# Performance work log

Hardware: AMD Instinct MI355X
Metric: run time of the kernel (lower is better)

The kernel has to match this reference:

```python
import jax, jax.numpy as jnp
import numpy as np

EPS = 1e-5
C_M, C, C_Z = 256, 32, 128
N_SEQ, N_RES = 256, 1024


def setup_inputs() -> dict:
    key = jax.random.key(0)
    k1, k2, k3 = jax.random.split(key, 3)
    msa = jax.random.normal(k1, (N_SEQ, N_RES, C_M), dtype=jnp.float32)
    norm_w = jnp.ones((C_M,), dtype=jnp.float32)
    norm_b = jnp.zeros((C_M,), dtype=jnp.float32)
    w_ab = jax.random.normal(k2, (C, C_M), dtype=jnp.float32) * (1.0 / np.sqrt(C_M))
    b_ab = jnp.zeros((C,), dtype=jnp.float32)
    w_out = jax.random.normal(k3, (C_Z, C * C), dtype=jnp.float32) * (1.0 / C)
    b_out = jnp.zeros((C_Z,), dtype=jnp.float32)
    return {"msa": msa, "norm_w": norm_w, "norm_b": norm_b,
            "w_ab": w_ab, "b_ab": b_ab, "w_out": w_out, "b_out": b_out}


def reference(msa, norm_w, norm_b, w_ab, b_ab, w_out, b_out):
    # msa: (s, r, c_m) -> (r, s, c_m)
    x = jnp.transpose(msa, (1, 0, 2))
    s = x.shape[1]
    # LayerNorm over c_m
    mu = jnp.mean(x, axis=-1, keepdims=True)
    var = jnp.mean(jnp.square(x - mu), axis=-1, keepdims=True)
    xn = (x - mu) * jax.lax.rsqrt(var + EPS) * norm_w + norm_b
    # a == b: same linear applied twice to same input in the original
    a = jnp.einsum('rsm,cm->rsc', xn, w_ab) + b_ab          # (r, s, c)
    # mean over s of outer product == batched A^T A / s  -> (r, c, c)
    o = jnp.einsum('rsx,rsy->rxy', a, a) / s
    o = o.reshape(o.shape[0], C * C)                        # (r, c*c)
    pre_pair = jnp.einsum('rk,zk->rz', o, w_out) + b_out    # (r, c_z)
    r = pre_pair.shape[0]
    # unsqueeze(1).expand(r, r, c_z)
    pair = jnp.broadcast_to(pre_pair[:, None, :], (r, r, C_Z))
    return pair
```

## Files before the change

kernel.cpp:

```cpp
#include <hip/hip_runtime.h>

#define NSEQ 256
#define NRES 1024
#define CM   256
#define CC   32
#define CZ   128
#define EPS  1e-5f
#define SROW (NRES * CM)

typedef float f4v __attribute__((ext_vector_type(4)));
typedef __attribute__((ext_vector_type(8))) short short8;
typedef __attribute__((ext_vector_type(4))) float f32x4;
typedef unsigned int u32;

__device__ __forceinline__ float trunc_bf16(float f) {
    return __uint_as_float(__float_as_uint(f) & 0xffff0000u);
}
__device__ __forceinline__ u32 pk_bf16(float a, float b) {
    return (__float_as_uint(b) & 0xffff0000u) | (__float_as_uint(a) >> 16);
}

__global__ void opm_setup(const float* __restrict__ nw,
                          const float* __restrict__ nb,
                          const float* __restrict__ w_ab,
                          const float* __restrict__ b_ab,
                          float* __restrict__ k12,
                          unsigned short* __restrict__ wb_su)
{
    __shared__ float wls[CM * CC];
    const int t = threadIdx.x;
    const float nwm = nw[t];
    #pragma unroll
    for (int c = 0; c < CC; ++c)
        wls[t * CC + c] = nwm * w_ab[c * CM + t];
    __syncthreads();
    if (t < CC) {
        float k1 = 0.f, k2 = 0.f;
        for (int m = 0; m < CM; ++m) {
            k1 += wls[m * CC + t];
            k2 = fmaf(nb[m], w_ab[t * CM + m], k2);
        }
        k12[t]      = k1;
        k12[CC + t] = k2 + b_ab[t];
    }
    for (int e = t; e < 16384; e += 256) {
        const int j     = e & 7;
        const int l     = (e >> 3) & 63;
        const int split = (e >> 9) & 1;
        const int nt    = (e >> 10) & 1;
        const int kk    = e >> 11;
        const int m = (kk << 5) + ((l >> 4) << 3) + j;
        const int c = (nt << 4) + (l & 15);
        const float w  = wls[m * CC + c];
        const float w1 = trunc_bf16(w);
        const float v  = split ? (w - w1) : w;
        wb_su[e] = (unsigned short)(__float_as_uint(v) >> 16);
    }
}

__launch_bounds__(256, 2)
__global__ void opm_compute(const float* __restrict__ msa,
                            const u32*  __restrict__ wb_g,
                            const float* __restrict__ k12,
                            const float* __restrict__ w_out,
                            const float* __restrict__ b_out,
                            float* __restrict__ pre_out)
{
    __shared__ u32 xp[2 * 5120];
    __shared__ u32 wbl[8192];
    __shared__ float st[520];

    const int tid = threadIdx.x;
    const int r   = blockIdx.x;
    const int w   = tid >> 6;
    const int l   = tid & 63;

    const int sc8 = tid & 7;
    const int sg8 = tid >> 3;
    const float* xr = msa + (size_t)r * CM + (sc8 << 2);

    u32* xp1 = xp;
    u32* xp2 = xp + 5120;

    #pragma unroll
    for (int k = 0; k < 8; ++k) {
        const int i = (tid + (k << 8)) << 2;
        *(f4v*)&wbl[i] = *(const f4v*)&wb_g[i];
    }

    f32x4 acc[4][2];
    #pragma unroll
    for (int mt = 0; mt < 4; ++mt) { acc[mt][0] = (f32x4)0.f; acc[mt][1] = (f32x4)0.f; }
    float psum[8], pssq[8];
    #pragma unroll
    for (int k = 0; k < 8; ++k) { psum[k] = 0.f; pssq[k] = 0.f; }

    float4 pf[8];
    #pragma unroll
    for (int k = 0; k < 8; ++k)
        pf[k] = *(const float4*)(xr + (size_t)(sg8 + (k << 5)) * SROW);

    for (int kk = 0; kk < 8; ++kk) {
        __syncthreads();
        #pragma unroll
        for (int k = 0; k < 8; ++k) {
            const float4 p = pf[k];
            const int row = sg8 + (k << 5);
            const u32 a0 = pk_bf16(p.x, p.y), a1 = pk_bf16(p.z, p.w);
            const float rx = p.x - trunc_bf16(p.x);
            const float ry = p.y - trunc_bf16(p.y);
            const float rz = p.z - trunc_bf16(p.z);
            const float rw = p.w - trunc_bf16(p.w);
            const u32 b0 = pk_bf16(rx, ry), b1 = pk_bf16(rz, rw);
            *(uint2*)&xp1[row * 20 + (sc8 << 1)] = make_uint2(a0, a1);
            *(uint2*)&xp2[row * 20 + (sc8 << 1)] = make_uint2(b0, b1);
            psum[k] += (p.x + p.y) + (p.z + p.w);
            pssq[k]  = fmaf(p.x, p.x, fmaf(p.y, p.y, fmaf(p.z, p.z, fmaf(p.w, p.w, pssq[k]))));
        }
        __syncthreads();
        if (kk < 7) {
            #pragma unroll
            for (int k = 0; k < 8; ++k)
                pf[k] = *(const float4*)(xr + (size_t)(sg8 + (k << 5)) * SROW + ((kk + 1) << 5));
        }
        short8 B[2][2];
        #pragma unroll
        for (int nt = 0; nt < 2; ++nt)
            #pragma unroll
            for (int sp = 0; sp < 2; ++sp) {
                const int fb = ((((kk << 1) + nt) << 1) + sp) * 256 + (l << 2);
                B[nt][sp] = __builtin_bit_cast(short8, *(const f4v*)&wbl[fb]);
            }
        #pragma unroll
        for (int mt = 0; mt < 4; ++mt) {
            const int arow = ((w << 6) + (mt << 4) + (l & 15)) * 20 + ((l >> 4) << 2);
            const short8 A1 = __builtin_bit_cast(short8, *(const f4v*)&xp1[arow]);
            const short8 A2 = __builtin_bit_cast(short8, *(const f4v*)&xp2[arow]);
            acc[mt][0] = __builtin_amdgcn_mfma_f32_16x16x32_bf16(A1, B[0][0], acc[mt][0], 0, 0, 0);
            acc[mt][1] = __builtin_amdgcn_mfma_f32_16x16x32_bf16(A1, B[1][0], acc[mt][1], 0, 0, 0);
            acc[mt][0] = __builtin_amdgcn_mfma_f32_16x16x32_bf16(A1, B[0][1], acc[mt][0], 0, 0, 0);
            acc[mt][1] = __builtin_amdgcn_mfma_f32_16x16x32_bf16(A1, B[1][1], acc[mt][1], 0, 0, 0);
            acc[mt][0] = __builtin_amdgcn_mfma_f32_16x16x32_bf16(A2, B[0][0], acc[mt][0], 0, 0, 0);
            acc[mt][1] = __builtin_amdgcn_mfma_f32_16x16x32_bf16(A2, B[1][0], acc[mt][1], 0, 0, 0);
        }
    }
    __syncthreads();

    #pragma unroll
    for (int k = 0; k < 8; ++k) {
        float s1 = psum[k], s2 = pssq[k];
        s1 += __shfl_xor(s1, 1); s1 += __shfl_xor(s1, 2); s1 += __shfl_xor(s1, 4);
        s2 += __shfl_xor(s2, 1); s2 += __shfl_xor(s2, 2); s2 += __shfl_xor(s2, 4);
        if (sc8 == 0) {
            const int s = sg8 + (k << 5);
            const float mu  = s1 * (1.f / CM);
            const float var = s2 * (1.f / CM) - mu * mu;
            st[s]        = mu;
            st[256 + s]  = 1.f / sqrtf(var + EPS);
        }
    }
    __syncthreads();

    float* aB = (float*)xp;
    {
        const int cl = l & 15;
        const float k1_0 = k12[cl],      k1_1 = k12[16 + cl];
        const float k2_0 = k12[CC + cl], k2_1 = k12[CC + 16 + cl];
        #pragma unroll
        for (int mt = 0; mt < 4; ++mt) {
            #pragma unroll
            for (int rg = 0; rg < 4; ++rg) {
                const int s = (w << 6) + (mt << 4) + ((l >> 4) << 2) + rg;
                const float mu = st[s], rs = st[256 + s];
                const float a0 = fmaf(rs, acc[mt][0][rg] - mu * k1_0, k2_0);
                const float a1 = fmaf(rs, acc[mt][1][rg] - mu * k1_1, k2_1);
                const int sw = s & 7;
                aB[s * CC + (((cl >> 2) ^ sw) << 2) + (cl & 3)]       = a0;
                aB[s * CC + ((((cl >> 2) + 4) ^ sw) << 2) + (cl & 3)] = a1;
            }
        }
    }
    __syncthreads();

    float* scr = (float*)wbl;
    const int grp = w;
    const int xs_ = (tid >> 3) & 7;
    const int ys_ = tid & 7;
    float4 pr0 = {0,0,0,0}, pr1 = {0,0,0,0}, pr2 = {0,0,0,0}, pr3 = {0,0,0,0};
    #pragma unroll 4
    for (int si = 0; si < 64; ++si) {
        const int s  = (grp << 6) + si;
        const int sw = s & 7;
        const float4 ax = *(const float4*)&aB[s * CC + ((xs_ ^ sw) << 2)];
        const float4 ay = *(const float4*)&aB[s * CC + ((ys_ ^ sw) << 2)];
        pr0.x = fmaf(ax.x, ay.x, pr0.x); pr0.y = fmaf(ax.x, ay.y, pr0.y);
        pr0.z = fmaf(ax.x, ay.z, pr0.z); pr0.w = fmaf(ax.x, ay.w, pr0.w);
        pr1.x = fmaf(ax.y, ay.x, pr1.x); pr1.y = fmaf(ax.y, ay.y, pr1.y);
        pr1.z = fmaf(ax.y, ay.z, pr1.z); pr1.w = fmaf(ax.y, ay.w, pr1.w);
        pr2.x = fmaf(ax.z, ay.x, pr2.x); pr2.y = fmaf(ax.z, ay.y, pr2.y);
        pr2.z = fmaf(ax.z, ay.z, pr2.z); pr2.w = fmaf(ax.z, ay.w, pr2.w);
        pr3.x = fmaf(ax.w, ay.x, pr3.x); pr3.y = fmaf(ax.w, ay.y, pr3.y);
        pr3.z = fmaf(ax.w, ay.z, pr3.z); pr3.w = fmaf(ax.w, ay.w, pr3.w);
    }
    {
        float* pb = &scr[(grp << 10) + ((xs_ << 2) * CC) + (ys_ << 2)];
        *(float4*)&pb[0 * CC] = pr0;
        *(float4*)&pb[1 * CC] = pr1;
        *(float4*)&pb[2 * CC] = pr2;
        *(float4*)&pb[3 * CC] = pr3;
    }
    __syncthreads();
    {
        const float inv_s = 1.f / NSEQ;
        float4 a4 = *(const float4*)&scr[(tid << 2)];
        const float4 b1 = *(const float4*)&scr[1024 + (tid << 2)];
        const float4 b2 = *(const float4*)&scr[2048 + (tid << 2)];
        const float4 b3 = *(const float4*)&scr[3072 + (tid << 2)];
        a4.x = (a4.x + b1.x + b2.x + b3.x) * inv_s;
        a4.y = (a4.y + b1.y + b2.y + b3.y) * inv_s;
        a4.z = (a4.z + b1.z + b2.z + b3.z) * inv_s;
        a4.w = (a4.w + b1.w + b2.w + b3.w) * inv_s;
        *(float4*)&scr[tid << 2] = a4;
    }
    __syncthreads();

    {
        const int z    = tid & 127;
        const int half = tid >> 7;
        const float* wrow = w_out + (size_t)z * (CC * CC) + half * 512;
        const float* op   = &scr[half * 512];
        float po = 0.f;
        #pragma unroll 8
        for (int k = 0; k < 512; k += 4) {
            const float4 o4 = *(const float4*)&op[k];
            const float4 w4 = *(const float4*)&wrow[k];
            po = fmaf(o4.x, w4.x, fmaf(o4.y, w4.y, fmaf(o4.z, w4.z, fmaf(o4.w, w4.w, po))));
        }
        scr[4096 + (half << 7) + z] = po;
    }
    __syncthreads();
    if (tid < CZ)
        pre_out[(size_t)r * CZ + tid] = scr[4096 + tid] + scr[4096 + CZ + tid] + b_out[tid];
}

__launch_bounds__(256, 8)
__global__ void opm_bcast(const float* __restrict__ pre,
                          float* __restrict__ out)
{
    const int bid = blockIdx.x;
    const int r   = bid >> 3;
    const int jb  = bid & 7;
    const int z4  = threadIdx.x & 31;
    const int jo  = threadIdx.x >> 5;

    const f4v pv = *((const f4v*)(pre + (size_t)r * CZ) + z4);
    f4v* outp = (f4v*)out + ((size_t)r * NRES + (size_t)jb * 128) * (CZ / 4);
    for (int j0 = 0; j0 < 128; j0 += 8)
        __builtin_nontemporal_store(pv, &outp[(size_t)(j0 + jo) * (CZ / 4) + z4]);
}

extern "C" void kernel_launch(void* const* d_in, const int* in_sizes, int n_in,
                              void* d_out, int out_size, void* d_ws, size_t ws_size,
                              hipStream_t stream) {
    const float* msa   = (const float*)d_in[0];
    const float* nw    = (const float*)d_in[1];
    const float* nb    = (const float*)d_in[2];
    const float* w_ab  = (const float*)d_in[3];
    const float* b_ab  = (const float*)d_in[4];
    const float* w_out = (const float*)d_in[5];
    const float* b_out = (const float*)d_in[6];
    float* out = (float*)d_out;

    float* pre = (float*)d_ws;
    float* k12 = pre + (size_t)NRES * CZ;
    unsigned short* wb_su = (unsigned short*)(k12 + 64);

    opm_setup<<<1, 256, 0, stream>>>(nw, nb, w_ab, b_ab, k12, wb_su);
    opm_compute<<<NRES, 256, 0, stream>>>(msa, (const u32*)wb_su, k12, w_out, b_out, pre);
    opm_bcast<<<NRES * 8, 256, 0, stream>>>(pre, out);
}
```

Baseline: 791.4 us.

## Load MSA directly into MFMA A-fragments, dropping LDS staging and per-chunk barriers

```diff
diff --git a/kernel.cpp b/kernel.cpp
--- a/kernel.cpp
+++ b/kernel.cpp
@@ -58,7 +58,7 @@
     }
 }
 
-__launch_bounds__(256, 2)
+__launch_bounds__(256, 3)
 __global__ void opm_compute(const float* __restrict__ msa,
                             const u32*  __restrict__ wb_g,
                             const float* __restrict__ k12,
@@ -66,21 +66,22 @@
                             const float* __restrict__ b_out,
                             float* __restrict__ pre_out)
 {
-    __shared__ u32 xp[2 * 5120];
     __shared__ u32 wbl[8192];
-    __shared__ float st[520];
+    __shared__ float scr[4352];
+    __shared__ float st[512];
 
     const int tid = threadIdx.x;
     const int r   = blockIdx.x;
     const int w   = tid >> 6;
     const int l   = tid & 63;
-
-    const int sc8 = tid & 7;
-    const int sg8 = tid >> 3;
-    const float* xr = msa + (size_t)r * CM + (sc8 << 2);
-
-    u32* xp1 = xp;
-    u32* xp2 = xp + 5120;
+    const int lr  = l & 15;
+    const int lk  = l >> 4;
+
+    const float* xr = msa + (size_t)r * CM;
+    size_t rowoff[4];
+    #pragma unroll
+    for (int mt = 0; mt < 4; ++mt)
+        rowoff[mt] = (size_t)((w << 6) + (mt << 4) + lr) * SROW + (lk << 3);
 
     #pragma unroll
     for (int k = 0; k < 8; ++k) {
@@ -91,37 +92,28 @@
     f32x4 acc[4][2];
     #pragma unroll
     for (int mt = 0; mt < 4; ++mt) { acc[mt][0] = (f32x4)0.f; acc[mt][1] = (f32x4)0.f; }
-    float psum[8], pssq[8];
-    #pragma unroll
-    for (int k = 0; k < 8; ++k) { psum[k] = 0.f; pssq[k] = 0.f; }
-
-    float4 pf[8];
-    #pragma unroll
-    for (int k = 0; k < 8; ++k)
-        pf[k] = *(const float4*)(xr + (size_t)(sg8 + (k << 5)) * SROW);
-
+    float psum[4], pssq[4];
+    #pragma unroll
+    for (int mt = 0; mt < 4; ++mt) { psum[mt] = 0.f; pssq[mt] = 0.f; }
+
+    float4 curA[4], curB[4], nxtA[4], nxtB[4];
+    #pragma unroll
+    for (int mt = 0; mt < 4; ++mt) {
+        curA[mt] = *(const float4*)(xr + rowoff[mt]);
+        curB[mt] = *(const float4*)(xr + rowoff[mt] + 4);
+    }
+
+    __syncthreads();
+
+    #pragma unroll 1
     for (int kk = 0; kk < 8; ++kk) {
-        __syncthreads();
-        #pragma unroll
-        for (int k = 0; k < 8; ++k) {
-            const float4 p = pf[k];
-            const int row = sg8 + (k << 5);
-            const u32 a0 = pk_bf16(p.x, p.y), a1 = pk_bf16(p.z, p.w);
-            const float rx = p.x - trunc_bf16(p.x);
-            const float ry = p.y - trunc_bf16(p.y);
-            const float rz = p.z - trunc_bf16(p.z);
-            const float rw = p.w - trunc_bf16(p.w);
-            const u32 b0 = pk_bf16(rx, ry), b1 = pk_bf16(rz, rw);
-            *(uint2*)&xp1[row * 20 + (sc8 << 1)] = make_uint2(a0, a1);
-            *(uint2*)&xp2[row * 20 + (sc8 << 1)] = make_uint2(b0, b1);
-            psum[k] += (p.x + p.y) + (p.z + p.w);
-            pssq[k]  = fmaf(p.x, p.x, fmaf(p.y, p.y, fmaf(p.z, p.z, fmaf(p.w, p.w, pssq[k]))));
-        }
-        __syncthreads();
         if (kk < 7) {
-            #pragma unroll
-            for (int k = 0; k < 8; ++k)
-                pf[k] = *(const float4*)(xr + (size_t)(sg8 + (k << 5)) * SROW + ((kk + 1) << 5));
+            const int o = (kk + 1) << 5;
+            #pragma unroll
+            for (int mt = 0; mt < 4; ++mt) {
+                nxtA[mt] = *(const float4*)(xr + rowoff[mt] + o);
+                nxtB[mt] = *(const float4*)(xr + rowoff[mt] + o + 4);
+            }
         }
         short8 B[2][2];
         #pragma unroll
@@ -133,9 +125,19 @@
             }
         #pragma unroll
         for (int mt = 0; mt < 4; ++mt) {
-            const int arow = ((w << 6) + (mt << 4) + (l & 15)) * 20 + ((l >> 4) << 2);
-            const short8 A1 = __builtin_bit_cast(short8, *(const f4v*)&xp1[arow]);
-            const short8 A2 = __builtin_bit_cast(short8, *(const f4v*)&xp2[arow]);
+            const float4 pa = curA[mt], pb = curB[mt];
+            psum[mt] += ((pa.x + pa.y) + (pa.z + pa.w)) + ((pb.x + pb.y) + (pb.z + pb.w));
+            pssq[mt]  = fmaf(pa.x, pa.x, fmaf(pa.y, pa.y, fmaf(pa.z, pa.z, fmaf(pa.w, pa.w, pssq[mt]))));
+            pssq[mt]  = fmaf(pb.x, pb.x, fmaf(pb.y, pb.y, fmaf(pb.z, pb.z, fmaf(pb.w, pb.w, pssq[mt]))));
+            uint4 u1, u2;
+            u1.x = pk_bf16(pa.x, pa.y); u1.y = pk_bf16(pa.z, pa.w);
+            u1.z = pk_bf16(pb.x, pb.y); u1.w = pk_bf16(pb.z, pb.w);
+            u2.x = pk_bf16(pa.x - trunc_bf16(pa.x), pa.y - trunc_bf16(pa.y));
+            u2.y = pk_bf16(pa.z - trunc_bf16(pa.z), pa.w - trunc_bf16(pa.w));
+            u2.z = pk_bf16(pb.x - trunc_bf16(pb.x), pb.y - trunc_bf16(pb.y));
+            u2.w = pk_bf16(pb.z - trunc_bf16(pb.z), pb.w - trunc_bf16(pb.w));
+            const short8 A1 = __builtin_bit_cast(short8, u1);
+            const short8 A2 = __builtin_bit_cast(short8, u2);
             acc[mt][0] = __builtin_amdgcn_mfma_f32_16x16x32_bf16(A1, B[0][0], acc[mt][0], 0, 0, 0);
             acc[mt][1] = __builtin_amdgcn_mfma_f32_16x16x32_bf16(A1, B[1][0], acc[mt][1], 0, 0, 0);
             acc[mt][0] = __builtin_amdgcn_mfma_f32_16x16x32_bf16(A1, B[0][1], acc[mt][0], 0, 0, 0);
@@ -143,34 +145,37 @@
             acc[mt][0] = __builtin_amdgcn_mfma_f32_16x16x32_bf16(A2, B[0][0], acc[mt][0], 0, 0, 0);
             acc[mt][1] = __builtin_amdgcn_mfma_f32_16x16x32_bf16(A2, B[1][0], acc[mt][1], 0, 0, 0);
         }
-    }
-    __syncthreads();
-
-    #pragma unroll
-    for (int k = 0; k < 8; ++k) {
-        float s1 = psum[k], s2 = pssq[k];
-        s1 += __shfl_xor(s1, 1); s1 += __shfl_xor(s1, 2); s1 += __shfl_xor(s1, 4);
-        s2 += __shfl_xor(s2, 1); s2 += __shfl_xor(s2, 2); s2 += __shfl_xor(s2, 4);
-        if (sc8 == 0) {
-            const int s = sg8 + (k << 5);
+        if (kk < 7) {
+            #pragma unroll
+            for (int mt = 0; mt < 4; ++mt) { curA[mt] = nxtA[mt]; curB[mt] = nxtB[mt]; }
+        }
+    }
+
+    #pragma unroll
+    for (int mt = 0; mt < 4; ++mt) {
+        float s1 = psum[mt], s2 = pssq[mt];
+        s1 += __shfl_xor(s1, 16); s1 += __shfl_xor(s1, 32);
+        s2 += __shfl_xor(s2, 16); s2 += __shfl_xor(s2, 32);
+        if (l < 16) {
+            const int s = (w << 6) + (mt << 4) + lr;
             const float mu  = s1 * (1.f / CM);
             const float var = s2 * (1.f / CM) - mu * mu;
-            st[s]        = mu;
-            st[256 + s]  = 1.f / sqrtf(var + EPS);
-        }
-    }
-    __syncthreads();
-
-    float* aB = (float*)xp;
-    {
-        const int cl = l & 15;
+            st[s]       = mu;
+            st[256 + s] = 1.f / sqrtf(var + EPS);
+        }
+    }
+    __syncthreads();
+
+    float* aB = (float*)wbl;
+    {
+        const int cl = lr;
         const float k1_0 = k12[cl],      k1_1 = k12[16 + cl];
         const float k2_0 = k12[CC + cl], k2_1 = k12[CC + 16 + cl];
         #pragma unroll
         for (int mt = 0; mt < 4; ++mt) {
             #pragma unroll
             for (int rg = 0; rg < 4; ++rg) {
-                const int s = (w << 6) + (mt << 4) + ((l >> 4) << 2) + rg;
+                const int s = (w << 6) + (mt << 4) + (lk << 2) + rg;
                 const float mu = st[s], rs = st[256 + s];
                 const float a0 = fmaf(rs, acc[mt][0][rg] - mu * k1_0, k2_0);
                 const float a1 = fmaf(rs, acc[mt][1][rg] - mu * k1_1, k2_1);
@@ -182,7 +187,6 @@
     }
     __syncthreads();
 
-    float* scr = (float*)wbl;
     const int grp = w;
     const int xs_ = (tid >> 3) & 7;
     const int ys_ = tid & 7;
```

Measured after the change: 789.0 us. About the same (-0.3%).
